# Kernel optimization log

Measured on AMD Instinct MI355X. Metric: run time of the kernel, lower is better.

The kernel has to match this reference:

```python
import jax, jax.numpy as jnp
import numpy as np
from jax import lax

B, T, E = 2, 2048, 2048
H, D = 16, 128
C = H * D          # qk_dim == v_dim == 2048
K = 4              # short conv kernel size
EPS = 1e-5


def setup_inputs() -> dict:
    key = jax.random.key(0)
    ks = jax.random.split(key, 11)
    s = 0.02
    return {
        "x": jax.random.normal(ks[0], (B, T, E), dtype=jnp.float32),
        "recurrent_state": jnp.zeros((B, H, D, D), dtype=jnp.float32),
        "Wq": jax.random.normal(ks[1], (C, E), dtype=jnp.float32) * s,
        "Wk": jax.random.normal(ks[2], (C, E), dtype=jnp.float32) * s,
        "Wv": jax.random.normal(ks[3], (C, E), dtype=jnp.float32) * s,
        "Wbeta": jax.random.normal(ks[4], (H, E), dtype=jnp.float32) * s,
        "Wgate": jax.random.normal(ks[5], (C, E), dtype=jnp.float32) * s,
        "Wo": jax.random.normal(ks[6], (E, C), dtype=jnp.float32) * s,
        "wq_conv": jax.random.normal(ks[7], (C, 1, K), dtype=jnp.float32) * 0.5,
        "wk_conv": jax.random.normal(ks[8], (C, 1, K), dtype=jnp.float32) * 0.5,
        "wv_conv": jax.random.normal(ks[9], (C, 1, K), dtype=jnp.float32) * 0.5,
    }


def _causal_dwconv(u, w):
    # u: (B, T, C), w: (C, 1, K). Torch pads both sides by K-1 then truncates
    # to length T -> equivalent to causal left-pad of K-1.
    u = u.transpose(0, 2, 1)  # (B, C, T)
    y = lax.conv_general_dilated(
        u, w, window_strides=(1,), padding=[(K - 1, 0)],
        feature_group_count=C, dimension_numbers=("NCH", "OIH", "NCH"))
    return y.transpose(0, 2, 1)  # (B, T, C)


def _delta_scan(q, k, v, beta, state):
    # q,k,v: (B,T,H,D); beta: (B,T,H); state: (B,H,D,D)
    def step(S, inp):
        qt, kt, vt, bt = inp  # (B,H,D),(B,H,D),(B,H,D),(B,H)
        b = bt[..., None, None]
        S = (1.0 - b) * S + b * (kt[..., :, None] * vt[..., None, :])  # bhde
        o = jnp.einsum("bhde,bhd->bhe", S, qt)
        return S, o

    xs = (q.transpose(1, 0, 2, 3), k.transpose(1, 0, 2, 3),
          v.transpose(1, 0, 2, 3), beta.transpose(1, 0, 2))
    final_state, outs = lax.scan(step, state, xs)
    return outs.transpose(1, 0, 2, 3), final_state  # (B,T,H,D)


def reference(x, recurrent_state, Wq, Wk, Wv, Wbeta, Wgate, Wo,
              wq_conv, wk_conv, wv_conv):
    q = jax.nn.silu(_causal_dwconv(x @ Wq.T, wq_conv))
    k = jax.nn.silu(_causal_dwconv(x @ Wk.T, wk_conv))
    v = jax.nn.silu(_causal_dwconv(x @ Wv.T, wv_conv))
    beta = jax.nn.sigmoid(x @ Wbeta.T)   # (B,T,H)
    gate = jax.nn.sigmoid(x @ Wgate.T)   # (B,T,C)

    q = q.reshape(B, T, H, D) * (D ** -0.5)
    k = k.reshape(B, T, H, D)
    v = v.reshape(B, T, H, D)

    out, new_state = _delta_scan(q, k, v, beta, recurrent_state)  # (B,T,H,D)

    # GroupNorm(num_groups=H, channels=C, affine=False) over (B, C, T):
    # normalizes each (batch, head) group over its (D, T) elements.
    mean = out.mean(axis=(1, 3), keepdims=True)
    var = out.var(axis=(1, 3), keepdims=True)
    out = (out - mean) * lax.rsqrt(var + EPS)

    out = out.reshape(B, T, C) * gate
    y = out @ Wo.T  # (B,T,E)
    return y, new_state
```

## Files before the change

### kernel.cpp

```cpp
#include <hip/hip_runtime.h>
#include <hip/hip_bf16.h>
#include <math.h>

#define BB 2
#define TT 2048
#define EE 2048
#define HH 16
#define DD 128
#define CC 2048
#define KCONV 4
#define CHUNK 128
#define NC 16
#define GN_EPS 1e-5f

typedef __bf16 bf16x8 __attribute__((ext_vector_type(8)));
typedef __bf16 bf16x4 __attribute__((ext_vector_type(4)));
typedef float  f32x4  __attribute__((ext_vector_type(4)));

#define GLD16(gp, lp)                                                          \
  __builtin_amdgcn_global_load_lds(                                            \
      (const __attribute__((address_space(1))) void*)(gp),                     \
      (__attribute__((address_space(3))) void*)(lp), 16, 0, 0)

__device__ __forceinline__ bf16x8 ldfrag(const __bf16* buf, int row, int kg)
{
  return *(const bf16x8*)(buf + row * 128 + ((kg ^ (row & 7)) << 3));
}

__global__ __launch_bounds__(256)
void convert_all(const float* __restrict__ x,  const float* __restrict__ Wq,
                 const float* __restrict__ Wk, const float* __restrict__ Wv,
                 const float* __restrict__ Wg, const float* __restrict__ Wo,
                 __bf16* __restrict__ xbf, __bf16* __restrict__ Wcat,
                 __bf16* __restrict__ Wob)
{
  const int i = (blockIdx.x * 256 + threadIdx.x) * 4;
  const int XN = 8388608, WN = 4194304;
  const float* src;
  __bf16* dst;
  int off;
  if (i < XN) { src = x; dst = xbf; off = i; }
  else if (i < XN + 4 * WN) {
    const int j = i - XN;
    const int seg = j >> 22;
    src = seg == 0 ? Wq : seg == 1 ? Wk : seg == 2 ? Wv : Wg;
    dst = Wcat + ((size_t)seg << 22);
    off = j & (WN - 1);
  } else { src = Wo; dst = Wob; off = i - XN - 4 * WN; }
  const float4 v = *(const float4*)(src + off);
  bf16x4 o;
  o[0] = (__bf16)v.x; o[1] = (__bf16)v.y; o[2] = (__bf16)v.z; o[3] = (__bf16)v.w;
  *(bf16x4*)(dst + off) = o;
}

__global__ __launch_bounds__(256)
void beta_ker(const float* __restrict__ x, const float* __restrict__ Wb,
              float* __restrict__ betab)
{
  __shared__ float wsb[16 * 1024];
  const int tid = threadIdx.x;
  const int w = tid >> 6, lane = tid & 63;
  const int row = blockIdx.x * 4 + w;
  const float* xrow = x + (size_t)row * EE;

  float acc[16] = {};
#pragma unroll
  for (int kt = 0; kt < 2; ++kt) {
    __syncthreads();
#pragma unroll
    for (int it = 0; it < 16; ++it) {
      const int i = tid + it * 256;
      const int h = i >> 8, kq = i & 255;
      *(float4*)&wsb[h * 1024 + kq * 4] =
          *(const float4*)(Wb + (size_t)h * EE + kt * 1024 + kq * 4);
    }
    __syncthreads();
#pragma unroll
    for (int j = 0; j < 4; ++j) {
      const int kof = lane * 4 + j * 256;
      const float4 xv = *(const float4*)(xrow + kt * 1024 + kof);
#pragma unroll
      for (int h = 0; h < 16; ++h) {
        const float4 wv = *(const float4*)&wsb[h * 1024 + kof];
        acc[h] += xv.x * wv.x + xv.y * wv.y + xv.z * wv.z + xv.w * wv.w;
      }
    }
  }
#pragma unroll
  for (int h = 0; h < 16; ++h) {
#pragma unroll
    for (int off = 32; off; off >>= 1)
      acc[h] += __shfl_xor(acc[h], off, 64);
  }
#pragma unroll
  for (int h = 0; h < 16; ++h)
    if (lane == h)
      betab[(size_t)row * HH + h] = 1.f / (1.f + expf(-acc[h]));
}

__global__ __launch_bounds__(512)
void gemm_big(const __bf16* __restrict__ A, const __bf16* __restrict__ Bm,
              __bf16* __restrict__ o0, __bf16* __restrict__ o1,
              __bf16* __restrict__ o2, __bf16* __restrict__ o3)
{
  __shared__ __attribute__((aligned(16))) unsigned char smem[163840];
  __bf16 (*ldsA)[256 * 64] = (__bf16(*)[256 * 64])smem;
  __bf16 (*ldsB)[256 * 64] = (__bf16(*)[256 * 64])(smem + 98304);

  const int tid = threadIdx.x;
  const int w = tid >> 6, l = tid & 63;
  const int wm = w >> 2, wn = w & 3;
  const int m0 = blockIdx.y * 256, n0 = blockIdx.x * 256;
  const int NT = EE / 64;

  const int sr0 = w * 8 + (l >> 3);
  const int skg = l & 7;
  const int fr = l & 15;
  const int fkg = l >> 4;

#define STAGE_A(tile, half) do {                                               \
    const int b_ = (tile) % 3;                                                 \
    const int r0_ = sr0;                                                       \
    const int r1_ = 64 + sr0;                                                  \
    GLD16(A + (size_t)(m0 + (half) * 128 + r0_) * 2048 + (tile) * 64           \
              + ((skg ^ (r0_ & 7)) << 3),                                      \
          ldsA[b_] + ((half) * 128 + w * 8) * 64);                             \
    GLD16(A + (size_t)(m0 + (half) * 128 + r1_) * 2048 + (tile) * 64           \
              + ((skg ^ (r1_ & 7)) << 3),                                      \
          ldsA[b_] + ((half) * 128 + 64 + w * 8) * 64);                        \
  } while (0)

#define STAGE_B(tile, half) do {                                               \
    const int b_ = (tile) & 1;                                                 \
    const int r0_ = sr0;                                                       \
    const int r1_ = 64 + sr0;                                                  \
    GLD16(Bm + (size_t)(n0 + (half) * 128 + r0_) * 2048 + (tile) * 64          \
              + ((skg ^ (r0_ & 7)) << 3),                                      \
          ldsB[b_] + ((half) * 128 + w * 8) * 64);                             \
    GLD16(Bm + (size_t)(n0 + (half) * 128 + r1_) * 2048 + (tile) * 64          \
              + ((skg ^ (r1_ & 7)) << 3),                                      \
          ldsB[b_] + ((half) * 128 + 64 + w * 8) * 64);                        \
  } while (0)

#define LDA_FRAG(dst, ab, q, mf, ks) do {                                      \
    const int row_ = wm * 128 + (q) * 32 + (mf) * 16 + fr;                     \
    const int kg_ = (ks) * 4 + fkg;                                            \
    dst = *(const bf16x8*)&ldsA[ab][row_ * 64 + ((kg_ ^ (row_ & 7)) << 3)];    \
  } while (0)
#define LDB_FRAG(dst, bb, nf, ks) do {                                         \
    const int row_ = wn * 64 + (nf) * 16 + fr;                                 \
    const int kg_ = (ks) * 4 + fkg;                                            \
    dst = *(const bf16x8*)&ldsB[bb][row_ * 64 + ((kg_ ^ (row_ & 7)) << 3)];    \
  } while (0)

  f32x4 acc[8][4] = {};

  STAGE_A(0, 0); STAGE_A(0, 1); STAGE_B(0, 0); STAGE_B(0, 1);
  STAGE_A(1, 0); STAGE_A(1, 1); STAGE_B(1, 0);
  asm volatile("s_waitcnt vmcnt(6)" ::: "memory");
  __builtin_amdgcn_s_barrier();

  for (int t = 0; t < NT; ++t) {
    const int abuf = t % 3;
    const int bbuf = t & 1;
    bf16x8 bfr[4][2];
    bf16x8 af[4][2];

#pragma unroll
    for (int nf = 0; nf < 4; ++nf)
#pragma unroll
      for (int ks = 0; ks < 2; ++ks) LDB_FRAG(bfr[nf][ks], bbuf, nf, ks);
#pragma unroll
    for (int q = 0; q < 2; ++q)
#pragma unroll
      for (int mf = 0; mf < 2; ++mf)
#pragma unroll
        for (int ks = 0; ks < 2; ++ks)
          LDA_FRAG(af[q * 2 + mf][ks], abuf, q, mf, ks);
    __builtin_amdgcn_s_barrier();
    if (t + 1 < NT) STAGE_B(t + 1, 1);
    if (t + 2 < NT) { STAGE_A(t + 2, 0); STAGE_A(t + 2, 1); }
    __builtin_amdgcn_s_setprio(1);
#pragma unroll
    for (int m2 = 0; m2 < 4; ++m2)
#pragma unroll
      for (int nf = 0; nf < 4; ++nf)
#pragma unroll
        for (int ks = 0; ks < 2; ++ks)
          acc[m2][nf] = __builtin_amdgcn_mfma_f32_16x16x32_bf16(
              af[m2][ks], bfr[nf][ks], acc[m2][nf], 0, 0, 0);
    __builtin_amdgcn_s_setprio(0);

#pragma unroll
    for (int q = 0; q < 2; ++q)
#pragma unroll
      for (int mf = 0; mf < 2; ++mf)
#pragma unroll
        for (int ks = 0; ks < 2; ++ks)
          LDA_FRAG(af[q * 2 + mf][ks], abuf, q + 2, mf, ks);
    if (t == NT - 2)     asm volatile("s_waitcnt vmcnt(0)" ::: "memory");
    else if (t < NT - 2) asm volatile("s_waitcnt vmcnt(4)" ::: "memory");
    __builtin_amdgcn_s_barrier();
    if (t + 2 < NT) STAGE_B(t + 2, 0);
    __builtin_amdgcn_s_setprio(1);
#pragma unroll
    for (int m2 = 0; m2 < 4; ++m2)
#pragma unroll
      for (int nf = 0; nf < 4; ++nf)
#pragma unroll
        for (int ks = 0; ks < 2; ++ks)
          acc[m2 + 4][nf] = __builtin_amdgcn_mfma_f32_16x16x32_bf16(
              af[m2][ks], bfr[nf][ks], acc[m2 + 4][nf], 0, 0, 0);
    __builtin_amdgcn_s_setprio(0);
  }

  __syncthreads();
  const int proj = n0 >> 11;
  const int nb = n0 & 2047;
  __bf16* outp = proj == 0 ? o0 : proj == 1 ? o1 : proj == 2 ? o2 : o3;
  __bf16* ep = (__bf16*)smem + (size_t)w * 9216;
  const int crow = (l >> 4) * 4;
#pragma unroll
  for (int mf2 = 0; mf2 < 8; ++mf2)
#pragma unroll
    for (int nf = 0; nf < 4; ++nf)
#pragma unroll
      for (int r = 0; r < 4; ++r) {
        const int row = mf2 * 16 + crow + r;
        float vv = acc[mf2][nf][r];
        if (proj == 3) vv = 1.f / (1.f + expf(-vv));
        ep[row * 72 + nf * 16 + fr] = (__bf16)vv;
      }
#pragma unroll
  for (int it = 0; it < 16; ++it) {
    const int row = it * 8 + (l >> 3);
    const int c8 = (l & 7) * 8;
    const bf16x8 v8 = *(const bf16x8*)&ep[row * 72 + c8];
    *(bf16x8*)(outp + (size_t)(m0 + wm * 128 + row) * 2048 + nb + wn * 64 + c8) = v8;
  }
#undef STAGE_A
#undef STAGE_B
#undef LDA_FRAG
#undef LDB_FRAG
}

__global__ __launch_bounds__(512)
void gemm_wo(const __bf16* __restrict__ A, const __bf16* __restrict__ Bm,
             float* __restrict__ Cm)
{
  __shared__ __attribute__((aligned(16))) unsigned char smem[147456];
  __bf16 (*ldsA)[128 * 64] = (__bf16(*)[128 * 64])smem;
  __bf16 (*ldsB)[256 * 64] = (__bf16(*)[256 * 64])(smem + 49152);

  const int tid = threadIdx.x;
  const int w = tid >> 6, l = tid & 63;
  const int wm = w >> 2, wn = w & 3;
  const int m0 = blockIdx.y * 128, n0 = blockIdx.x * 256;
  const int NT = CC / 64;

  const int sr0 = w * 8 + (l >> 3);
  const int skg = l & 7;
  const int fr = l & 15;
  const int fkg = l >> 4;

#define STAGE_AW(tile) do {                                                    \
    const int b_ = (tile) % 3;                                                 \
    const int r0_ = sr0;                                                       \
    const int r1_ = 64 + sr0;                                                  \
    GLD16(A + (size_t)(m0 + r0_) * 2048 + (tile) * 64                          \
              + ((skg ^ (r0_ & 7)) << 3),                                      \
          ldsA[b_] + (w * 8) * 64);                                            \
    GLD16(A + (size_t)(m0 + r1_) * 2048 + (tile) * 64                          \
              + ((skg ^ (r1_ & 7)) << 3),                                      \
          ldsA[b_] + (64 + w * 8) * 64);                                       \
  } while (0)

#define STAGE_BW(tile, half) do {                                              \
    const int b_ = (tile) % 3;                                                 \
    const int r0_ = sr0;                                                       \
    const int r1_ = 64 + sr0;                                                  \
    GLD16(Bm + (size_t)(n0 + (half) * 128 + r0_) * 2048 + (tile) * 64          \
              + ((skg ^ (r0_ & 7)) << 3),                                      \
          ldsB[b_] + ((half) * 128 + w * 8) * 64);                             \
    GLD16(Bm + (size_t)(n0 + (half) * 128 + r1_) * 2048 + (tile) * 64          \
              + ((skg ^ (r1_ & 7)) << 3),                                      \
          ldsB[b_] + ((half) * 128 + 64 + w * 8) * 64);                        \
  } while (0)

#define LDA_FRAGW(dst, ab, mf, ks) do {                                        \
    const int row_ = wm * 64 + (mf) * 16 + fr;                                 \
    const int kg_ = (ks) * 4 + fkg;                                            \
    dst = *(const bf16x8*)&ldsA[ab][row_ * 64 + ((kg_ ^ (row_ & 7)) << 3)];    \
  } while (0)
#define LDB_FRAGW(dst, bb, nf, ks) do {                                        \
    const int row_ = wn * 64 + (nf) * 16 + fr;                                 \
    const int kg_ = (ks) * 4 + fkg;                                            \
    dst = *(const bf16x8*)&ldsB[bb][row_ * 64 + ((kg_ ^ (row_ & 7)) << 3)];    \
  } while (0)

  f32x4 acc[4][4] = {};

  STAGE_BW(0, 0); STAGE_BW(0, 1); STAGE_AW(0);
  STAGE_BW(1, 0); STAGE_BW(1, 1); STAGE_AW(1);

  for (int t = 0; t < NT; ++t) {
    const int buf = t % 3;
    bf16x8 bfr[4][2];
    bf16x8 af[4][2];

    if (t == NT - 1) asm volatile("s_waitcnt vmcnt(0)" ::: "memory");
    else             asm volatile("s_waitcnt vmcnt(6)" ::: "memory");
    __builtin_amdgcn_s_barrier();

#pragma unroll
    for (int nf = 0; nf < 4; ++nf)
#pragma unroll
      for (int ks = 0; ks < 2; ++ks) LDB_FRAGW(bfr[nf][ks], buf, nf, ks);
#pragma unroll
    for (int mf = 0; mf < 4; ++mf)
#pragma unroll
      for (int ks = 0; ks < 2; ++ks) LDA_FRAGW(af[mf][ks], buf, mf, ks);

    if (t + 2 < NT) { STAGE_BW(t + 2, 0); STAGE_BW(t + 2, 1); STAGE_AW(t + 2); }

    __builtin_amdgcn_s_setprio(1);
#pragma unroll
    for (int mf = 0; mf < 4; ++mf)
#pragma unroll
      for (int nf = 0; nf < 4; ++nf)
#pragma unroll
        for (int ks = 0; ks < 2; ++ks)
          acc[mf][nf] = __builtin_amdgcn_mfma_f32_16x16x32_bf16(
              af[mf][ks], bfr[nf][ks], acc[mf][nf], 0, 0, 0);
    __builtin_amdgcn_s_setprio(0);
  }

  __syncthreads();
  float* ep = (float*)smem + (size_t)w * (64 * 68);
  const int crow = (l >> 4) * 4;
#pragma unroll
  for (int mf = 0; mf < 4; ++mf)
#pragma unroll
    for (int nf = 0; nf < 4; ++nf)
#pragma unroll
      for (int r = 0; r < 4; ++r)
        ep[(mf * 16 + crow + r) * 68 + nf * 16 + fr] = acc[mf][nf][r];
#pragma unroll
  for (int it = 0; it < 16; ++it) {
    const int row = it * 4 + (l >> 4);
    const int c4 = (l & 15) * 4;
    const float4 v4 = *(const float4*)&ep[row * 68 + c4];
    *(float4*)(Cm + (size_t)(m0 + wm * 64 + row) * 2048 + n0 + wn * 64 + c4) = v4;
  }
#undef STAGE_AW
#undef STAGE_BW
#undef LDA_FRAGW
#undef LDB_FRAGW
}

__global__ __launch_bounds__(256)
void conv_tr(const __bf16* __restrict__ u_q, const __bf16* __restrict__ u_k,
             const __bf16* __restrict__ u_v, const float* __restrict__ wq,
             const float* __restrict__ wk, const float* __restrict__ wv,
             __bf16* __restrict__ qbf, __bf16* __restrict__ kbf,
             __bf16* __restrict__ kT, __bf16* __restrict__ vT, float qscale)
{
  const int t0 = blockIdx.x * 64, c0 = blockIdx.y * 64;
  const int which = blockIdx.z / BB, b = blockIdx.z % BB;
  const __bf16* u = which == 0 ? u_q : which == 1 ? u_k : u_v;
  const float* wc = which == 0 ? wq : which == 1 ? wk : wv;
  const float scale = which == 0 ? qscale : 1.f;
  const int tid = threadIdx.x;
  __shared__ __attribute__((aligned(16))) __bf16 tile[64][72];

#pragma unroll
  for (int it = 0; it < 2; ++it) {
    const int idx = tid + it * 256;
    const int tl = idx >> 3, g = idx & 7;
    const int t = t0 + tl;
    const int c8 = c0 + g * 8;
    const size_t base = ((size_t)(b * TT + t)) * CC + c8;
    const bf16x8 z = {};
    const bf16x8 uu0 = *(const bf16x8*)(u + base);
    const bf16x8 uu1 = (t >= 1) ? *(const bf16x8*)(u + base - CC)     : z;
    const bf16x8 uu2 = (t >= 2) ? *(const bf16x8*)(u + base - 2 * CC) : z;
    const bf16x8 uu3 = (t >= 3) ? *(const bf16x8*)(u + base - 3 * CC) : z;
    bf16x8 o;
#pragma unroll
    for (int jj = 0; jj < 8; ++jj) {
      const float4 wv4 = *(const float4*)(wc + (size_t)(c8 + jj) * 4);
      const float vv = wv4.x * (float)uu3[jj] + wv4.y * (float)uu2[jj]
                     + wv4.z * (float)uu1[jj] + wv4.w * (float)uu0[jj];
      o[jj] = (__bf16)(vv / (1.f + expf(-vv)) * scale);
    }
    if (which == 0) *(bf16x8*)(qbf + base) = o;
    if (which == 1) *(bf16x8*)(kbf + base) = o;
    if (which >= 1) *(bf16x8*)&tile[tl][g * 8] = o;
  }
  if (which >= 1) {
    __syncthreads();
    const int h = c0 >> 7, d0 = c0 & 127;
    const int bh = b * HH + h;
    __bf16* dst = (which == 1) ? kT : vT;
#pragma unroll
    for (int it = 0; it < 2; ++it) {
      const int idx = tid + it * 256;
      const int dl = idx >> 3, g = idx & 7;
      bf16x8 o;
#pragma unroll
      for (int jj = 0; jj < 8; ++jj) o[jj] = tile[g * 8 + jj][dl];
      *(bf16x8*)(dst + ((size_t)(bh * DD + d0 + dl)) * TT + t0 + g * 8) = o;
    }
  }
}

__global__ __launch_bounds__(256)
void phaseA_mfma(const __bf16* __restrict__ kT, const __bf16* __restrict__ vT,
                 const float* __restrict__ beta, float* __restrict__ contribT,
                 float* __restrict__ decay)
{
  const int c = blockIdx.x, h = blockIdx.y, b = blockIdx.z;
  const int bh = b * HH + h;
  const int tid = threadIdx.x;
  const int w = tid >> 6, lane = tid & 63;
  const int wm = w >> 1, wn = w & 1;

  __shared__ __attribute__((aligned(16))) __bf16 bufVT[128 * 128];
  __shared__ __attribute__((aligned(16))) __bf16 bufKW[128 * 128];
  __shared__ float lc[CHUNK], bsh[CHUNK], wgt[CHUNK];

  {
    const __bf16* vbase = vT + ((size_t)bh * DD) * TT + c * CHUNK;
#pragma unroll
    for (int jj = 0; jj < 8; ++jj) {
      const int row = w * 32 + jj * 4 + (lane >> 4);
      const int g = lane & 15;
      GLD16(vbase + (size_t)row * TT + ((g ^ (row & 7)) << 3),
            bufVT + (w * 32 + jj * 4) * 128);
    }
  }

  if (tid < CHUNK) {
    const float bv = beta[(size_t)(b * TT + c * CHUNK + tid) * HH + h];
    bsh[tid] = bv;
    lc[tid] = log1pf(-bv);
  }
  __syncthreads();
  for (int off = 1; off < CHUNK; off <<= 1) {
    float add = 0.f;
    if (tid < CHUNK && tid >= off) add = lc[tid - off];
    __syncthreads();
    if (tid < CHUNK) lc[tid] += add;
    __syncthreads();
  }
  const float lend = lc[CHUNK - 1];
  if (tid < CHUNK) wgt[tid] = bsh[tid] * expf(lend - lc[tid]);
  if (tid == 0) decay[(size_t)bh * NC + c] = expf(lend);
  __syncthreads();

  {
    const __bf16* kbase = kT + ((size_t)bh * DD) * TT + c * CHUNK;
#pragma unroll
    for (int it = 0; it < 8; ++it) {
      const int idx = tid + it * 256;
      const int d = idx >> 4, g = idx & 15;
      const bf16x8 kv = *(const bf16x8*)(kbase + (size_t)d * TT + g * 8);
      bf16x8 o;
#pragma unroll
      for (int jj = 0; jj < 8; ++jj)
        o[jj] = (__bf16)((float)kv[jj] * wgt[g * 8 + jj]);
      *(bf16x8*)(bufKW + d * 128 + ((g ^ (d & 7)) << 3)) = o;
    }
  }
  asm volatile("s_waitcnt vmcnt(0)" ::: "memory");
  __syncthreads();

  f32x4 acc[4][4] = {};
#pragma unroll
  for (int ks = 0; ks < 4; ++ks) {
    bf16x8 a[4], bq[4];
    const int kg = ks * 4 + (lane >> 4);
#pragma unroll
    for (int f = 0; f < 4; ++f) a[f]  = ldfrag(bufVT, wm * 64 + f * 16 + (lane & 15), kg);
#pragma unroll
    for (int f = 0; f < 4; ++f) bq[f] = ldfrag(bufKW, wn * 64 + f * 16 + (lane & 15), kg);
#pragma unroll
    for (int i = 0; i < 4; ++i)
#pragma unroll
      for (int j = 0; j < 4; ++j)
        acc[i][j] = __builtin_amdgcn_mfma_f32_16x16x32_bf16(a[i], bq[j], acc[i][j], 0, 0, 0);
  }

  float* cp = contribT + ((size_t)(bh * NC + c) << 14);
  const int crow = (lane >> 4) * 4;
#pragma unroll
  for (int i = 0; i < 4; ++i)
#pragma unroll
    for (int j = 0; j < 4; ++j) {
      const int dd = wn * 64 + j * 16 + (lane & 15);
#pragma unroll
      for (int r = 0; r < 4; ++r) {
        const int e = wm * 64 + i * 16 + crow + r;
        cp[(size_t)e * 128 + dd] = acc[i][j][r];
      }
    }
}

__global__ __launch_bounds__(256)
void phaseB_T(const float* __restrict__ st0, const float* __restrict__ contribT,
              const float* __restrict__ decay, __bf16* __restrict__ statesT,
              float* __restrict__ stOut)
{
  const size_t gid = (size_t)blockIdx.x * 256 + threadIdx.x;
  const int bh = (int)(gid >> 14);
  const int ed = (int)(gid & 16383);
  const int e = ed >> 7, d = ed & 127;
  const size_t tidx = ((size_t)bh << 14) + (size_t)d * 128 + e;
  float s = st0[tidx];
  const float* dc = decay + (size_t)bh * NC;
#pragma unroll
  for (int c = 0; c < NC; ++c) {
    const size_t off = ((size_t)(bh * NC + c) << 14) + ed;
    statesT[off] = (__bf16)s;
    s = fmaf(dc[c], s, contribT[off]);
  }
  stOut[tidx] = s;
}

__global__ __launch_bounds__(256)
void phaseC_mfma(const __bf16* __restrict__ qb, const __bf16* __restrict__ kb,
                 const __bf16* __restrict__ vT, const float* __restrict__ beta,
                 const __bf16* __restrict__ statesT, float* __restrict__ att,
                 float* __restrict__ partials)
{
  const int c = blockIdx.x, h = blockIdx.y, b = blockIdx.z;
  const int bh = b * HH + h;
  const int tid = threadIdx.x;
  const int w = tid >> 6, lane = tid & 63;
  const int wm = w >> 1, wn = w & 1;

  __shared__ __attribute__((aligned(16))) __bf16 bufQ[128 * 128];
  __shared__ __attribute__((aligned(16))) __bf16 bufB[128 * 128];
  __shared__ float lc[CHUNK], bsh[CHUNK];
  __shared__ float s1[256], s2[256];

  {
    const __bf16* qbase = qb + ((size_t)(b * TT + c * CHUNK)) * CC + h * DD;
    const __bf16* kbase = kb + ((size_t)(b * TT + c * CHUNK)) * CC + h * DD;
#pragma unroll
    for (int jj = 0; jj < 8; ++jj) {
      const int row = w * 32 + jj * 4 + (lane >> 4);
      const int g = lane & 15;
      GLD16(qbase + (size_t)row * CC + ((g ^ (row & 7)) << 3),
            bufQ + (w * 32 + jj * 4) * 128);
      GLD16(kbase + (size_t)row * CC + ((g ^ (row & 7)) << 3),
            bufB + (w * 32 + jj * 4) * 128);
    }
  }

  if (tid < CHUNK) {
    const float bv = beta[(size_t)(b * TT + c * CHUNK + tid) * HH + h];
    bsh[tid] = bv;
    lc[tid] = log1pf(-bv);
  }
  __syncthreads();
  for (int off = 1; off < CHUNK; off <<= 1) {
    float add = 0.f;
    if (tid < CHUNK && tid >= off) add = lc[tid - off];
    __syncthreads();
    if (tid < CHUNK) lc[tid] += add;
    __syncthreads();
  }

  asm volatile("s_waitcnt vmcnt(0)" ::: "memory");
  __syncthreads();

  f32x4 accS[4][4] = {};
#pragma unroll
  for (int ks = 0; ks < 4; ++ks) {
    bf16x8 a[4], bq[4];
    const int kg = ks * 4 + (lane >> 4);
#pragma unroll
    for (int f = 0; f < 4; ++f) a[f]  = ldfrag(bufQ, wm * 64 + f * 16 + (lane & 15), kg);
#pragma unroll
    for (int f = 0; f < 4; ++f) bq[f] = ldfrag(bufB, wn * 64 + f * 16 + (lane & 15), kg);
#pragma unroll
    for (int i = 0; i < 4; ++i)
#pragma unroll
      for (int j = 0; j < 4; ++j)
        accS[i][j] = __builtin_amdgcn_mfma_f32_16x16x32_bf16(a[i], bq[j], accS[i][j], 0, 0, 0);
  }

  __syncthreads();
  {
    const __bf16* sbase = statesT + ((size_t)(bh * NC + c) << 14);
#pragma unroll
    for (int jj = 0; jj < 8; ++jj) {
      const int row = w * 32 + jj * 4 + (lane >> 4);
      const int g = lane & 15;
      GLD16(sbase + (size_t)row * 128 + ((g ^ (row & 7)) << 3),
            bufB + (w * 32 + jj * 4) * 128);
    }
  }
  asm volatile("s_waitcnt vmcnt(0)" ::: "memory");
  __syncthreads();

  f32x4 accO[4][4] = {};
#pragma unroll
  for (int ks = 0; ks < 4; ++ks) {
    bf16x8 a[4], bq[4];
    const int kg = ks * 4 + (lane >> 4);
#pragma unroll
    for (int f = 0; f < 4; ++f) a[f]  = ldfrag(bufQ, wm * 64 + f * 16 + (lane & 15), kg);
#pragma unroll
    for (int f = 0; f < 4; ++f) bq[f] = ldfrag(bufB, wn * 64 + f * 16 + (lane & 15), kg);
#pragma unroll
    for (int i = 0; i < 4; ++i)
#pragma unroll
      for (int j = 0; j < 4; ++j)
        accO[i][j] = __builtin_amdgcn_mfma_f32_16x16x32_bf16(a[i], bq[j], accO[i][j], 0, 0, 0);
  }
  const int crow = (lane >> 4) * 4;
#pragma unroll
  for (int i = 0; i < 4; ++i)
#pragma unroll
    for (int r = 0; r < 4; ++r) {
      const float el = expf(lc[wm * 64 + i * 16 + crow + r]);
#pragma unroll
      for (int j = 0; j < 4; ++j) accO[i][j][r] *= el;
    }

  __syncthreads();
  {
    const __bf16* vbase = vT + ((size_t)bh * DD) * TT + c * CHUNK;
#pragma unroll
    for (int jj = 0; jj < 8; ++jj) {
      const int row = w * 32 + jj * 4 + (lane >> 4);
      const int g = lane & 15;
      GLD16(vbase + (size_t)row * TT + ((g ^ (row & 7)) << 3),
            bufB + (w * 32 + jj * 4) * 128);
    }
  }
  {
    float lcs[4], bss[4];
#pragma unroll
    for (int j = 0; j < 4; ++j) {
      const int s = wn * 64 + j * 16 + (lane & 15);
      lcs[j] = lc[s]; bss[j] = bsh[s];
    }
#pragma unroll
    for (int i = 0; i < 4; ++i)
#pragma unroll
      for (int r = 0; r < 4; ++r) {
        const int t = wm * 64 + i * 16 + crow + r;
        const float lct = lc[t];
#pragma unroll
        for (int j = 0; j < 4; ++j) {
          const int s = wn * 64 + j * 16 + (lane & 15);
          float p = 0.f;
          if (s <= t) p = accS[i][j][r] * bss[j] * expf(lct - lcs[j]);
          bufQ[t * 128 + (((s >> 3) ^ (t & 7)) << 3) + (s & 7)] = (__bf16)p;
        }
      }
  }
  asm volatile("s_waitcnt vmcnt(0)" ::: "memory");
  __syncthreads();

#pragma unroll
  for (int ks = 0; ks < 4; ++ks) {
    bf16x8 a[4], bq[4];
    const int kg = ks * 4 + (lane >> 4);
#pragma unroll
    for (int f = 0; f < 4; ++f) a[f]  = ldfrag(bufQ, wm * 64 + f * 16 + (lane & 15), kg);
#pragma unroll
    for (int f = 0; f < 4; ++f) bq[f] = ldfrag(bufB, wn * 64 + f * 16 + (lane & 15), kg);
#pragma unroll
    for (int i = 0; i < 4; ++i)
#pragma unroll
      for (int j = 0; j < 4; ++j)
        accO[i][j] = __builtin_amdgcn_mfma_f32_16x16x32_bf16(a[i], bq[j], accO[i][j], 0, 0, 0);
  }

  float lsum = 0.f, lsq = 0.f;
  float* obase = att + ((size_t)(b * TT + c * CHUNK)) * CC + h * DD;
#pragma unroll
  for (int i = 0; i < 4; ++i)
#pragma unroll
    for (int j = 0; j < 4; ++j) {
      const int e = wn * 64 + j * 16 + (lane & 15);
#pragma unroll
      for (int r = 0; r < 4; ++r) {
        const int t = wm * 64 + i * 16 + crow + r;
        const float vv = accO[i][j][r];
        obase[(size_t)t * CC + e] = vv;
        lsum += vv;
        lsq  += vv * vv;
      }
    }
  s1[tid] = lsum; s2[tid] = lsq;
  __syncthreads();
  for (int off = 128; off; off >>= 1) {
    if (tid < off) { s1[tid] += s1[tid + off]; s2[tid] += s2[tid + off]; }
    __syncthreads();
  }
  if (tid == 0) {
    partials[(size_t)(bh * NC + c) * 2]     = s1[0];
    partials[(size_t)(bh * NC + c) * 2 + 1] = s2[0];
  }
}

__global__ __launch_bounds__(256)
void norm_gate(const float* __restrict__ att, const __bf16* __restrict__ gate,
               const float* __restrict__ partials, __bf16* __restrict__ g)
{
  __shared__ float sm[8], sr[8];
  const int tid = threadIdx.x;
  const size_t gid0 = (size_t)blockIdx.x * 1024;
  const int b = (int)(gid0 >> 22);
  const int h0 = ((int)(gid0 & 2047)) >> 7;
  if (tid < 8) {
    const int bh = b * HH + h0 + tid;
    float s = 0.f, q = 0.f;
#pragma unroll
    for (int cc = 0; cc < NC; ++cc) {
      s += partials[(size_t)(bh * NC + cc) * 2];
      q += partials[(size_t)(bh * NC + cc) * 2 + 1];
    }
    const float n = (float)(TT * DD);
    const float mean = s / n;
    sm[tid] = mean;
    sr[tid] = rsqrtf(q / n - mean * mean + GN_EPS);
  }
  __syncthreads();
  const size_t gid = gid0 + (size_t)tid * 4;
  const int hl = (tid * 4) >> 7;
  const float mean = sm[hl], rstd = sr[hl];
  const float4 a = *(const float4*)(att + gid);
  const bf16x4 gt = *(const bf16x4*)(gate + gid);
  bf16x4 o;
  o[0] = (__bf16)((a.x - mean) * rstd * (float)gt[0]);
  o[1] = (__bf16)((a.y - mean) * rstd * (float)gt[1]);
  o[2] = (__bf16)((a.z - mean) * rstd * (float)gt[2]);
  o[3] = (__bf16)((a.w - mean) * rstd * (float)gt[3]);
  *(bf16x4*)(g + gid) = o;
}

extern "C" void kernel_launch(void* const* d_in, const int* in_sizes, int n_in,
                              void* d_out, int out_size, void* d_ws, size_t ws_size,
                              hipStream_t stream)
{
  const float* x      = (const float*)d_in[0];
  const float* st0    = (const float*)d_in[1];
  const float* Wq     = (const float*)d_in[2];
  const float* Wk     = (const float*)d_in[3];
  const float* Wv     = (const float*)d_in[4];
  const float* Wbeta  = (const float*)d_in[5];
  const float* Wgate  = (const float*)d_in[6];
  const float* Wo     = (const float*)d_in[7];
  const float* wqc    = (const float*)d_in[8];
  const float* wkc    = (const float*)d_in[9];
  const float* wvc    = (const float*)d_in[10];

  float* ws = (float*)d_ws;
  __bf16* qbf  = (__bf16*)(ws + 0);
  __bf16* kbf  = (__bf16*)(ws + 4194304);
  __bf16* u_v  = (__bf16*)(ws + 8388608);
  __bf16* statesT = (__bf16*)(ws + 8388608);
  __bf16* kT   = (__bf16*)(ws + 12582912);
  __bf16* gbf  = (__bf16*)(ws + 12582912);
  __bf16* vT   = (__bf16*)(ws + 16777216);
  __bf16* xbf  = (__bf16*)(ws + 20971520);
  float* contribT = ws + 20971520;
  __bf16* Wcat = (__bf16*)(ws + 25165824);
  __bf16* gatebuf = (__bf16*)(ws + 33554432);
  float* betab    = ws + 37748736;
  float* decay    = ws + 37814272;
  float* partials = ws + 37814848;
  __bf16* Wob  = (__bf16*)(ws + 38864448);

  float* y_out  = (float*)d_out;
  float* st_out = (float*)d_out + (size_t)BB * TT * EE;
  __bf16* u_q = (__bf16*)d_out;
  __bf16* u_k = (__bf16*)d_out + 8388608;
  float* att = y_out;

  const dim3 blk(256);
  const dim3 gBig(8192 / 256, (BB * TT) / 256);
  const dim3 gWo(EE / 256, (BB * TT) / 128);
  const dim3 gConv(TT / 64, CC / 64, 3 * BB);
  const dim3 gScan(NC, HH, BB);
  const float qscale = 0.08838834764831845f;

  convert_all<<<dim3(28672), blk, 0, stream>>>(x, Wq, Wk, Wv, Wgate, Wo,
                                               xbf, Wcat, Wob);

  beta_ker<<<dim3((BB * TT) / 4), blk, 0, stream>>>(x, Wbeta, betab);

  gemm_big<<<gBig, dim3(512), 0, stream>>>(xbf, Wcat, u_q, u_k, u_v, gatebuf);

  conv_tr<<<gConv, blk, 0, stream>>>(u_q, u_k, u_v, wqc, wkc, wvc,
                                     qbf, kbf, kT, vT, qscale);

  phaseA_mfma<<<gScan, blk, 0, stream>>>(kT, vT, betab, contribT, decay);
  phaseB_T<<<dim3((BB * HH * DD * DD) / 256), blk, 0, stream>>>(st0, contribT, decay, statesT, st_out);
  phaseC_mfma<<<gScan, blk, 0, stream>>>(qbf, kbf, vT, betab, statesT, att, partials);

  norm_gate<<<dim3((BB * TT * CC) / 1024), blk, 0, stream>>>(att, gatebuf, partials, gbf);

  gemm_wo<<<gWo, dim3(512), 0, stream>>>(gbf, Wob, y_out);
}
```

Measured before the change: 333.0 us.

## Split projection GEMM main loop into four interleaved load/MFMA phases

The projection GEMM k-loop is restructured from two halves into four phases. Each phase loads only the A fragments for one 32-row quarter, issues one slice of global-to-LDS staging, waits, and runs 16 MFMAs. Explicit lgkmcnt waits and sched_barriers pin the ordering. The aim is to spread global loads across the loop and cut A-fragment register pressure, which may raise overlap. The cost is twice as many workgroup barriers per iteration, which can stall the waves.

```diff
diff --git a/kernel.cpp b/kernel.cpp
--- a/kernel.cpp
+++ b/kernel.cpp
@@ -153,6 +153,19 @@
     dst = *(const bf16x8*)&ldsB[bb][row_ * 64 + ((kg_ ^ (row_ & 7)) << 3)];    \
   } while (0)
 
+#define MFMA16(Q) do {                                                         \
+    __builtin_amdgcn_s_setprio(1);                                             \
+    _Pragma("unroll")                                                          \
+    for (int mf = 0; mf < 2; ++mf)                                             \
+      _Pragma("unroll")                                                        \
+      for (int nf = 0; nf < 4; ++nf)                                           \
+        _Pragma("unroll")                                                      \
+        for (int ks = 0; ks < 2; ++ks)                                         \
+          acc[2 * (Q) + mf][nf] = __builtin_amdgcn_mfma_f32_16x16x32_bf16(     \
+              af[mf][ks], bfr[nf][ks], acc[2 * (Q) + mf][nf], 0, 0, 0);        \
+    __builtin_amdgcn_s_setprio(0);                                             \
+  } while (0)
+
   f32x4 acc[8][4] = {};
 
   STAGE_A(0, 0); STAGE_A(0, 1); STAGE_B(0, 0); STAGE_B(0, 1);
@@ -164,54 +177,69 @@
     const int abuf = t % 3;
     const int bbuf = t & 1;
     bf16x8 bfr[4][2];
-    bf16x8 af[4][2];
-
-#pragma unroll
-    for (int nf = 0; nf < 4; ++nf)
-#pragma unroll
-      for (int ks = 0; ks < 2; ++ks) LDB_FRAG(bfr[nf][ks], bbuf, nf, ks);
-#pragma unroll
-    for (int q = 0; q < 2; ++q)
+
+    {
+      bf16x8 af[2][2];
+#pragma unroll
+      for (int nf = 0; nf < 4; ++nf)
+#pragma unroll
+        for (int ks = 0; ks < 2; ++ks) LDB_FRAG(bfr[nf][ks], bbuf, nf, ks);
 #pragma unroll
       for (int mf = 0; mf < 2; ++mf)
 #pragma unroll
-        for (int ks = 0; ks < 2; ++ks)
-          LDA_FRAG(af[q * 2 + mf][ks], abuf, q, mf, ks);
-    __builtin_amdgcn_s_barrier();
-    if (t + 1 < NT) STAGE_B(t + 1, 1);
-    if (t + 2 < NT) { STAGE_A(t + 2, 0); STAGE_A(t + 2, 1); }
-    __builtin_amdgcn_s_setprio(1);
-#pragma unroll
-    for (int m2 = 0; m2 < 4; ++m2)
-#pragma unroll
-      for (int nf = 0; nf < 4; ++nf)
-#pragma unroll
-        for (int ks = 0; ks < 2; ++ks)
-          acc[m2][nf] = __builtin_amdgcn_mfma_f32_16x16x32_bf16(
-              af[m2][ks], bfr[nf][ks], acc[m2][nf], 0, 0, 0);
-    __builtin_amdgcn_s_setprio(0);
-
-#pragma unroll
-    for (int q = 0; q < 2; ++q)
+        for (int ks = 0; ks < 2; ++ks) LDA_FRAG(af[mf][ks], abuf, 0, mf, ks);
+      if (t + 1 < NT) STAGE_B(t + 1, 1);
+      asm volatile("s_waitcnt lgkmcnt(8)" ::: "memory");
+      __builtin_amdgcn_s_barrier();
+      asm volatile("s_waitcnt lgkmcnt(0)" ::: "memory");
+      __builtin_amdgcn_sched_barrier(0);
+      MFMA16(0);
+      __builtin_amdgcn_s_barrier();
+    }
+
+    {
+      bf16x8 af[2][2];
 #pragma unroll
       for (int mf = 0; mf < 2; ++mf)
 #pragma unroll
-        for (int ks = 0; ks < 2; ++ks)
-          LDA_FRAG(af[q * 2 + mf][ks], abuf, q + 2, mf, ks);
-    if (t == NT - 2)     asm volatile("s_waitcnt vmcnt(0)" ::: "memory");
-    else if (t < NT - 2) asm volatile("s_waitcnt vmcnt(4)" ::: "memory");
-    __builtin_amdgcn_s_barrier();
-    if (t + 2 < NT) STAGE_B(t + 2, 0);
-    __builtin_amdgcn_s_setprio(1);
-#pragma unroll
-    for (int m2 = 0; m2 < 4; ++m2)
-#pragma unroll
-      for (int nf = 0; nf < 4; ++nf)
-#pragma unroll
-        for (int ks = 0; ks < 2; ++ks)
-          acc[m2 + 4][nf] = __builtin_amdgcn_mfma_f32_16x16x32_bf16(
-              af[m2][ks], bfr[nf][ks], acc[m2 + 4][nf], 0, 0, 0);
-    __builtin_amdgcn_s_setprio(0);
+        for (int ks = 0; ks < 2; ++ks) LDA_FRAG(af[mf][ks], abuf, 1, mf, ks);
+      if (t + 2 < NT) STAGE_A(t + 2, 0);
+      __builtin_amdgcn_s_barrier();
+      asm volatile("s_waitcnt lgkmcnt(0)" ::: "memory");
+      __builtin_amdgcn_sched_barrier(0);
+      MFMA16(1);
+      __builtin_amdgcn_s_barrier();
+    }
+
+    {
+      bf16x8 af[2][2];
+#pragma unroll
+      for (int mf = 0; mf < 2; ++mf)
+#pragma unroll
+        for (int ks = 0; ks < 2; ++ks) LDA_FRAG(af[mf][ks], abuf, 2, mf, ks);
+      if (t + 2 < NT) STAGE_A(t + 2, 1);
+      __builtin_amdgcn_s_barrier();
+      asm volatile("s_waitcnt lgkmcnt(0)" ::: "memory");
+      __builtin_amdgcn_sched_barrier(0);
+      MFMA16(2);
+      __builtin_amdgcn_s_barrier();
+    }
+
+    {
+      bf16x8 af[2][2];
+#pragma unroll
+      for (int mf = 0; mf < 2; ++mf)
+#pragma unroll
+        for (int ks = 0; ks < 2; ++ks) LDA_FRAG(af[mf][ks], abuf, 3, mf, ks);
+      if (t + 2 < NT) STAGE_B(t + 2, 0);
+      if (t == NT - 2)     asm volatile("s_waitcnt vmcnt(0)" ::: "memory");
+      else if (t < NT - 2) asm volatile("s_waitcnt vmcnt(6)" ::: "memory");
+      __builtin_amdgcn_s_barrier();
+      asm volatile("s_waitcnt lgkmcnt(0)" ::: "memory");
+      __builtin_amdgcn_sched_barrier(0);
+      MFMA16(3);
+      __builtin_amdgcn_s_barrier();
+    }
   }
 
   __syncthreads();
@@ -242,6 +270,7 @@
 #undef STAGE_B
 #undef LDA_FRAG
 #undef LDB_FRAG
+#undef MFMA16
 }
 
 __global__ __launch_bounds__(512)
```

Result: no change. 335.9 us (+0.9%).

## Fuse x bf16 conversion into beta kernel, swizzle GEMM tiles, finer pipeline

Applied to the files above, without the earlier changes.

The x-to-bf16 conversion moves into the beta kernel, which already reads x, so the separate pass no longer reads x a second time. Both GEMMs remap block indices with a swizzle so that consecutive blocks share A/B tiles, aiming for better L2 (infinity cache) reuse. gemm_big's main loop is split into four sub-phases of 2 M-fragments each, with loads interleaved between them and a waitcnt adjusted to 6. This lowers fragment register pressure and spreads memory issue more evenly, at the cost of more barriers per K-tile.

```diff
diff --git a/kernel.cpp b/kernel.cpp
--- a/kernel.cpp
+++ b/kernel.cpp
@@ -28,25 +28,22 @@
 }
 
 __global__ __launch_bounds__(256)
-void convert_all(const float* __restrict__ x,  const float* __restrict__ Wq,
-                 const float* __restrict__ Wk, const float* __restrict__ Wv,
-                 const float* __restrict__ Wg, const float* __restrict__ Wo,
-                 __bf16* __restrict__ xbf, __bf16* __restrict__ Wcat,
-                 __bf16* __restrict__ Wob)
+void convert_w(const float* __restrict__ Wq, const float* __restrict__ Wk,
+               const float* __restrict__ Wv, const float* __restrict__ Wg,
+               const float* __restrict__ Wo, __bf16* __restrict__ Wcat,
+               __bf16* __restrict__ Wob)
 {
   const int i = (blockIdx.x * 256 + threadIdx.x) * 4;
-  const int XN = 8388608, WN = 4194304;
+  const int WN = 4194304;
   const float* src;
   __bf16* dst;
   int off;
-  if (i < XN) { src = x; dst = xbf; off = i; }
-  else if (i < XN + 4 * WN) {
-    const int j = i - XN;
-    const int seg = j >> 22;
+  if (i < 4 * WN) {
+    const int seg = i >> 22;
     src = seg == 0 ? Wq : seg == 1 ? Wk : seg == 2 ? Wv : Wg;
     dst = Wcat + ((size_t)seg << 22);
-    off = j & (WN - 1);
-  } else { src = Wo; dst = Wob; off = i - XN - 4 * WN; }
+    off = i & (WN - 1);
+  } else { src = Wo; dst = Wob; off = i - 4 * WN; }
   const float4 v = *(const float4*)(src + off);
   bf16x4 o;
   o[0] = (__bf16)v.x; o[1] = (__bf16)v.y; o[2] = (__bf16)v.z; o[3] = (__bf16)v.w;
@@ -55,13 +52,14 @@
 
 __global__ __launch_bounds__(256)
 void beta_ker(const float* __restrict__ x, const float* __restrict__ Wb,
-              float* __restrict__ betab)
+              float* __restrict__ betab, __bf16* __restrict__ xbf)
 {
   __shared__ float wsb[16 * 1024];
   const int tid = threadIdx.x;
   const int w = tid >> 6, lane = tid & 63;
   const int row = blockIdx.x * 4 + w;
   const float* xrow = x + (size_t)row * EE;
+  __bf16* xbrow = xbf + (size_t)row * EE;
 
   float acc[16] = {};
 #pragma unroll
@@ -79,6 +77,10 @@
     for (int j = 0; j < 4; ++j) {
       const int kof = lane * 4 + j * 256;
       const float4 xv = *(const float4*)(xrow + kt * 1024 + kof);
+      bf16x4 xb;
+      xb[0] = (__bf16)xv.x; xb[1] = (__bf16)xv.y;
+      xb[2] = (__bf16)xv.z; xb[3] = (__bf16)xv.w;
+      *(bf16x4*)(xbrow + kt * 1024 + kof) = xb;
 #pragma unroll
       for (int h = 0; h < 16; ++h) {
         const float4 wv = *(const float4*)&wsb[h * 1024 + kof];
@@ -110,7 +112,9 @@
   const int tid = threadIdx.x;
   const int w = tid >> 6, l = tid & 63;
   const int wm = w >> 2, wn = w & 3;
-  const int m0 = blockIdx.y * 256, n0 = blockIdx.x * 256;
+  const int orig = blockIdx.x + (blockIdx.y << 5);
+  const int swz = (orig & 7) * 64 + (orig >> 3);
+  const int m0 = (swz & 15) * 256, n0 = (swz >> 4) * 256;
   const int NT = EE / 64;
 
   const int sr0 = w * 8 + (l >> 3);
@@ -164,54 +168,59 @@
     const int abuf = t % 3;
     const int bbuf = t & 1;
     bf16x8 bfr[4][2];
-    bf16x8 af[4][2];
-
-#pragma unroll
-    for (int nf = 0; nf < 4; ++nf)
-#pragma unroll
-      for (int ks = 0; ks < 2; ++ks) LDB_FRAG(bfr[nf][ks], bbuf, nf, ks);
-#pragma unroll
-    for (int q = 0; q < 2; ++q)
+
+    {
+      bf16x8 af[2][2];
+#pragma unroll
+      for (int nf = 0; nf < 4; ++nf)
+#pragma unroll
+        for (int ks = 0; ks < 2; ++ks) LDB_FRAG(bfr[nf][ks], bbuf, nf, ks);
 #pragma unroll
       for (int mf = 0; mf < 2; ++mf)
 #pragma unroll
-        for (int ks = 0; ks < 2; ++ks)
-          LDA_FRAG(af[q * 2 + mf][ks], abuf, q, mf, ks);
-    __builtin_amdgcn_s_barrier();
-    if (t + 1 < NT) STAGE_B(t + 1, 1);
-    if (t + 2 < NT) { STAGE_A(t + 2, 0); STAGE_A(t + 2, 1); }
-    __builtin_amdgcn_s_setprio(1);
-#pragma unroll
-    for (int m2 = 0; m2 < 4; ++m2)
-#pragma unroll
-      for (int nf = 0; nf < 4; ++nf)
-#pragma unroll
-        for (int ks = 0; ks < 2; ++ks)
-          acc[m2][nf] = __builtin_amdgcn_mfma_f32_16x16x32_bf16(
-              af[m2][ks], bfr[nf][ks], acc[m2][nf], 0, 0, 0);
-    __builtin_amdgcn_s_setprio(0);
-
-#pragma unroll
-    for (int q = 0; q < 2; ++q)
+        for (int ks = 0; ks < 2; ++ks) LDA_FRAG(af[mf][ks], abuf, 0, mf, ks);
+      if (t + 1 < NT) STAGE_B(t + 1, 1);
+      __builtin_amdgcn_s_barrier();
+      __builtin_amdgcn_s_setprio(1);
 #pragma unroll
       for (int mf = 0; mf < 2; ++mf)
 #pragma unroll
-        for (int ks = 0; ks < 2; ++ks)
-          LDA_FRAG(af[q * 2 + mf][ks], abuf, q + 2, mf, ks);
-    if (t == NT - 2)     asm volatile("s_waitcnt vmcnt(0)" ::: "memory");
-    else if (t < NT - 2) asm volatile("s_waitcnt vmcnt(4)" ::: "memory");
-    __builtin_amdgcn_s_barrier();
-    if (t + 2 < NT) STAGE_B(t + 2, 0);
-    __builtin_amdgcn_s_setprio(1);
-#pragma unroll
-    for (int m2 = 0; m2 < 4; ++m2)
-#pragma unroll
-      for (int nf = 0; nf < 4; ++nf)
-#pragma unroll
-        for (int ks = 0; ks < 2; ++ks)
-          acc[m2 + 4][nf] = __builtin_amdgcn_mfma_f32_16x16x32_bf16(
-              af[m2][ks], bfr[nf][ks], acc[m2 + 4][nf], 0, 0, 0);
-    __builtin_amdgcn_s_setprio(0);
+        for (int nf = 0; nf < 4; ++nf)
+#pragma unroll
+          for (int ks = 0; ks < 2; ++ks)
+            acc[mf][nf] = __builtin_amdgcn_mfma_f32_16x16x32_bf16(
+                af[mf][ks], bfr[nf][ks], acc[mf][nf], 0, 0, 0);
+      __builtin_amdgcn_s_setprio(0);
+    }
+
+#pragma unroll
+    for (int q = 1; q < 4; ++q) {
+      bf16x8 af[2][2];
+#pragma unroll
+      for (int mf = 0; mf < 2; ++mf)
+#pragma unroll
+        for (int ks = 0; ks < 2; ++ks) LDA_FRAG(af[mf][ks], abuf, q, mf, ks);
+      if (q == 1) {
+        if (t + 2 < NT) STAGE_A(t + 2, 0);
+      } else if (q == 2) {
+        if (t + 2 < NT) STAGE_A(t + 2, 1);
+      } else {
+        if (t + 2 < NT) STAGE_B(t + 2, 0);
+        if (t == NT - 2)     asm volatile("s_waitcnt vmcnt(0)" ::: "memory");
+        else if (t < NT - 2) asm volatile("s_waitcnt vmcnt(6)" ::: "memory");
+      }
+      __builtin_amdgcn_s_barrier();
+      __builtin_amdgcn_s_setprio(1);
+#pragma unroll
+      for (int mf = 0; mf < 2; ++mf)
+#pragma unroll
+        for (int nf = 0; nf < 4; ++nf)
+#pragma unroll
+          for (int ks = 0; ks < 2; ++ks)
+            acc[2 * q + mf][nf] = __builtin_amdgcn_mfma_f32_16x16x32_bf16(
+                af[mf][ks], bfr[nf][ks], acc[2 * q + mf][nf], 0, 0, 0);
+      __builtin_amdgcn_s_setprio(0);
+    }
   }
 
   __syncthreads();
@@ -255,7 +264,9 @@
   const int tid = threadIdx.x;
   const int w = tid >> 6, l = tid & 63;
   const int wm = w >> 2, wn = w & 3;
-  const int m0 = blockIdx.y * 128, n0 = blockIdx.x * 256;
+  const int orig = blockIdx.x + (blockIdx.y << 3);
+  const int swz = (orig & 7) * 32 + (orig >> 3);
+  const int m0 = (swz & 31) * 128, n0 = (swz >> 5) * 256;
   const int NT = CC / 64;
 
   const int sr0 = w * 8 + (l >> 3);
@@ -791,10 +802,9 @@
   const dim3 gScan(NC, HH, BB);
   const float qscale = 0.08838834764831845f;
 
-  convert_all<<<dim3(28672), blk, 0, stream>>>(x, Wq, Wk, Wv, Wgate, Wo,
-                                               xbf, Wcat, Wob);
-
-  beta_ker<<<dim3((BB * TT) / 4), blk, 0, stream>>>(x, Wbeta, betab);
+  convert_w<<<dim3(20480), blk, 0, stream>>>(Wq, Wk, Wv, Wgate, Wo, Wcat, Wob);
+
+  beta_ker<<<dim3((BB * TT) / 4), blk, 0, stream>>>(x, Wbeta, betab, xbf);
 
   gemm_big<<<gBig, dim3(512), 0, stream>>>(xbf, Wcat, u_q, u_k, u_v, gatebuf);
 
```

Measured after the change: 334.8 us. About the same (+0.5%).
